# Performance work log

Hardware: AMD Instinct MI355X
Metric: run time of the kernel (lower is better)

Reference implementation:

```python
import jax, jax.numpy as jnp
import numpy as np

D = 768
N_ATOM = 1000 + 1   # num_atom_templates + 1
N_BOND = 300 + 1    # num_bond_templates + 1


def setup_inputs() -> dict:
    key = jax.random.key(0)
    k1, k2, k3, k4, k5 = jax.random.split(key, 5)
    scale = 1.0 / np.sqrt(D)
    return {
        "input_states": jax.random.normal(k1, (8, 256, D), dtype=jnp.float32),
        "Wa": jax.random.normal(k2, (N_ATOM, D), dtype=jnp.float32) * scale,
        "ba": jax.random.normal(k3, (N_ATOM,), dtype=jnp.float32) * 0.01,
        "Wb": jax.random.normal(k4, (N_BOND, 2 * D), dtype=jnp.float32) * scale,
        "bb": jax.random.normal(k5, (N_BOND,), dtype=jnp.float32) * 0.01,
    }


def reference(input_states, Wa, ba, Wb, bb):
    # Atom head: [B, L, n_a]
    atom_logits = jnp.einsum("bld,ad->bla", input_states, Wa) + ba

    # Bond head. Original math: linear(cat(x_i, x_j)) over all pairs (i, j).
    # Since Linear(cat(x_i, x_j)) = x_i @ W1.T + x_j @ W2.T + b with
    # W1 = Wb[:, :D], W2 = Wb[:, D:], we project once per token and
    # broadcast-add, avoiding the O(L^2 * 2D) concat intermediate.
    W1 = Wb[:, :D]
    W2 = Wb[:, D:]
    p1 = jnp.einsum("bld,nd->bln", input_states, W1)  # [B, L, n_b]
    p2 = jnp.einsum("bld,nd->bln", input_states, W2)  # [B, L, n_b]
    bond_logits = p1[:, :, None, :] + p2[:, None, :, :] + bb  # [B, L, L, n_b]

    return (atom_logits, bond_logits)
```

## Files before the change

kernel.cpp:

```cpp
#include <hip/hip_runtime.h>

#define DK      768
#define M_ROWS  2048
#define N_ATOM  1001
#define N_BOND  301
#define N_TOT   1603
#define N_PADR  1664
#define ATOM_ELEMS 2050048
#define P_ELEMS    616448
#define SLAB_F4    19264

typedef __attribute__((ext_vector_type(4))) float f32x4;
typedef __attribute__((ext_vector_type(8))) short bf16x8;

static __device__ __forceinline__ unsigned short f2bf(float f) {
    unsigned u = __float_as_uint(f);
    u += 0x7FFFu + ((u >> 16) & 1u);
    return (unsigned short)(u >> 16);
}

static __device__ __forceinline__ void gload_lds16(const void* g, void* l) {
    __builtin_amdgcn_global_load_lds(
        (const __attribute__((address_space(1))) unsigned*)g,
        (__attribute__((address_space(3))) unsigned*)l, 16, 0, 0);
}

__global__ __launch_bounds__(256) void pack_bf16(
    const float* __restrict__ x, const float* __restrict__ Wa,
    const float* __restrict__ Wb,
    ushort* __restrict__ xb, ushort* __restrict__ wcat)
{
    const int NX4 = (M_ROWS * DK) / 4;
    const int NW4 = (N_PADR * DK) / 4;
    int t = blockIdx.x * 256 + threadIdx.x;
    if (t < NX4) {
        float4 v = ((const float4*)x)[t];
        ushort4 o;
        o.x = f2bf(v.x); o.y = f2bf(v.y); o.z = f2bf(v.z); o.w = f2bf(v.w);
        ((ushort4*)xb)[t] = o;
    } else if (t < NX4 + NW4) {
        int u = t - NX4;
        int r = u / 192;
        int c = (u - r * 192) * 4;
        float4 v = make_float4(0.f, 0.f, 0.f, 0.f);
        if (r < N_ATOM) {
            v = *(const float4*)(Wa + (size_t)r * DK + c);
        } else if (r < N_TOT) {
            int q = r - N_ATOM;
            v = *(const float4*)(Wb + (size_t)(q >> 1) * (2 * DK) + (q & 1) * DK + c);
        }
        ushort4 o;
        o.x = f2bf(v.x); o.y = f2bf(v.y); o.z = f2bf(v.z); o.w = f2bf(v.w);
        ((ushort4*)wcat)[u] = o;
    }
}

__global__ __launch_bounds__(256) void gemm_mfma(
    const ushort* __restrict__ xb, const ushort* __restrict__ wcat,
    const float* __restrict__ ba, const float* __restrict__ bb,
    float* __restrict__ atom, float* __restrict__ p1, float* __restrict__ p2)
{
    __shared__ char As[8192];
    __shared__ char Bs[8192];

    const int tid  = threadIdx.x;
    const int lane = tid & 63;
    const int wid  = tid >> 6;
    const int wr   = wid >> 1;
    const int wc   = wid & 1;
    const int m0   = blockIdx.y * 64;
    const int n0   = blockIdx.x * 64;

    f32x4 acc[2][2] = {};

    const int lrow = lane >> 3;
    const int lcx  = ((lane & 7) ^ lrow) * 8;

    const ushort* Ag = xb   + (size_t)m0 * DK;
    const ushort* Bg = wcat + (size_t)n0 * DK;

    for (int k0 = 0; k0 < DK; k0 += 64) {
        __syncthreads();
        #pragma unroll
        for (int t = 0; t < 2; ++t) {
            const int s = wid + 4 * t;
            gload_lds16(Ag + (size_t)(s * 8 + lrow) * DK + k0 + lcx, As + s * 1024);
            gload_lds16(Bg + (size_t)(s * 8 + lrow) * DK + k0 + lcx, Bs + s * 1024);
        }
        __syncthreads();
        #pragma unroll
        for (int ks = 0; ks < 2; ++ks) {
            const int kc = ks * 4 + (lane >> 4);
            bf16x8 af[2], bfr[2];
            #pragma unroll
            for (int i = 0; i < 2; ++i) {
                int ra = wr * 32 + i * 16 + (lane & 15);
                af[i]  = *(const bf16x8*)(As + ra * 128 + ((kc ^ (ra & 7)) << 4));
                int rb = wc * 32 + i * 16 + (lane & 15);
                bfr[i] = *(const bf16x8*)(Bs + rb * 128 + ((kc ^ (rb & 7)) << 4));
            }
            #pragma unroll
            for (int i = 0; i < 2; ++i)
                #pragma unroll
                for (int j = 0; j < 2; ++j)
                    acc[i][j] = __builtin_amdgcn_mfma_f32_16x16x32_bf16(
                        af[i], bfr[j], acc[i][j], 0, 0, 0);
        }
    }

    #pragma unroll
    for (int i = 0; i < 2; ++i) {
        #pragma unroll
        for (int j = 0; j < 2; ++j) {
            #pragma unroll
            for (int reg = 0; reg < 4; ++reg) {
                int m = m0 + wr * 32 + i * 16 + (lane >> 4) * 4 + reg;
                int n = n0 + wc * 32 + j * 16 + (lane & 15);
                float v = acc[i][j][reg];
                if (n < N_ATOM) {
                    atom[(size_t)m * N_ATOM + n] = v + ba[n];
                } else if (n < N_TOT) {
                    int q = n - N_ATOM, rr = q >> 1;
                    if (q & 1) p2[(size_t)m * N_BOND + rr] = v + bb[rr];
                    else       p1[(size_t)m * N_BOND + rr] = v;
                }
            }
        }
    }
}

__global__ __launch_bounds__(256) void bond_bcast(
    const float* __restrict__ p1, const float* __restrict__ p2,
    f32x4* __restrict__ out)
{
    __shared__ float p1s[344];
    const int bi  = blockIdx.x;
    const int b   = bi >> 8;
    const int tid = threadIdx.x;

    for (int n = tid; n < N_BOND; n += 256)
        p1s[n + (n >> 3)] = p1[(size_t)bi * N_BOND + n];
    __syncthreads();

    const f32x4* p2f = (const f32x4*)(p2 + (size_t)(b << 8) * N_BOND);
    f32x4* of = out + (size_t)bi * SLAB_F4;

    int n = (4 * tid) % 301;
    for (int f = tid; f < SLAB_F4; f += 256) {
        f32x4 v = p2f[f];
        int n0 = n;
        int n1 = n + 1; if (n1 >= 301) n1 -= 301;
        int n2 = n + 2; if (n2 >= 301) n2 -= 301;
        int n3 = n + 3; if (n3 >= 301) n3 -= 301;
        v.x += p1s[n0 + (n0 >> 3)];
        v.y += p1s[n1 + (n1 >> 3)];
        v.z += p1s[n2 + (n2 >> 3)];
        v.w += p1s[n3 + (n3 >> 3)];
        of[f] = v;
        n += 121; if (n >= 301) n -= 301;
    }
}

extern "C" void kernel_launch(void* const* d_in, const int* in_sizes, int n_in,
                              void* d_out, int out_size, void* d_ws, size_t ws_size,
                              hipStream_t stream) {
    const float* x  = (const float*)d_in[0];
    const float* Wa = (const float*)d_in[1];
    const float* ba = (const float*)d_in[2];
    const float* Wb = (const float*)d_in[3];
    const float* bb = (const float*)d_in[4];

    float* out  = (float*)d_out;
    float* atom = out;
    float* bond = out + ATOM_ELEMS;

    ushort* xb   = (ushort*)d_ws;
    ushort* wcat = xb + (size_t)M_ROWS * DK;
    float*  p1   = (float*)(wcat + (size_t)N_PADR * DK);
    float*  p2   = p1 + P_ELEMS;

    pack_bf16<<<dim3(2784), dim3(256), 0, stream>>>(x, Wa, Wb, xb, wcat);

    gemm_mfma<<<dim3(N_PADR / 64, M_ROWS / 64), dim3(256), 0, stream>>>(
        xb, wcat, ba, bb, atom, p1, p2);

    bond_bcast<<<dim3(2048), dim3(256), 0, stream>>>(p1, p2, (f32x4*)bond);
}
```

Before: 183.0 us.

## Tile bond broadcast over 32x16 token pairs with both projections staged in LDS

The bond broadcast kernel now gives each block a 32-row by 16-column tile of (i, j) token pairs. It stages the matching p1 and p2 rows in shared memory, so the full per-batch p2 slab is no longer re-read from global/L2 for every output row. Output is written as coalesced scalar floats across 32 consecutive slab rows, and the grid shrinks to 1024 blocks. In exchange it uses about 58KB of LDS per block, which limits occupancy, and it drops the 16-byte vector stores in a kernel that is dominated by writes.

New measurement: 159.8 us. 1.15x faster.

```diff
diff --git a/kernel.cpp b/kernel.cpp
--- a/kernel.cpp
+++ b/kernel.cpp
@@ -8,7 +8,7 @@
 #define N_PADR  1664
 #define ATOM_ELEMS 2050048
 #define P_ELEMS    616448
-#define SLAB_F4    19264
+#define SLAB       77056
 
 typedef __attribute__((ext_vector_type(4))) float f32x4;
 typedef __attribute__((ext_vector_type(8))) short bf16x8;
@@ -131,33 +131,34 @@
 
 __global__ __launch_bounds__(256) void bond_bcast(
     const float* __restrict__ p1, const float* __restrict__ p2,
-    f32x4* __restrict__ out)
+    float* __restrict__ out)
 {
-    __shared__ float p1s[344];
-    const int bi  = blockIdx.x;
-    const int b   = bi >> 8;
+    __shared__ float p1s[32 * N_BOND];
+    __shared__ float p2s[16 * N_BOND];
+    const int blk = blockIdx.x;
+    const int b   = blk >> 7;
+    const int it  = (blk >> 4) & 7;
+    const int jt  = blk & 15;
     const int tid = threadIdx.x;
 
-    for (int n = tid; n < N_BOND; n += 256)
-        p1s[n + (n >> 3)] = p1[(size_t)bi * N_BOND + n];
+    const f32x4* p1g = (const f32x4*)(p1 + (size_t)(b * 256 + it * 32) * N_BOND);
+    const f32x4* p2g = (const f32x4*)(p2 + (size_t)(b * 256 + jt * 16) * N_BOND);
+    for (int k = tid; k < 2408; k += 256) ((f32x4*)p1s)[k] = p1g[k];
+    for (int k = tid; k < 1204; k += 256) ((f32x4*)p2s)[k] = p2g[k];
     __syncthreads();
 
-    const f32x4* p2f = (const f32x4*)(p2 + (size_t)(b << 8) * N_BOND);
-    f32x4* of = out + (size_t)bi * SLAB_F4;
-
-    int n = (4 * tid) % 301;
-    for (int f = tid; f < SLAB_F4; f += 256) {
-        f32x4 v = p2f[f];
-        int n0 = n;
-        int n1 = n + 1; if (n1 >= 301) n1 -= 301;
-        int n2 = n + 2; if (n2 >= 301) n2 -= 301;
-        int n3 = n + 3; if (n3 >= 301) n3 -= 301;
-        v.x += p1s[n0 + (n0 >> 3)];
-        v.y += p1s[n1 + (n1 >> 3)];
-        v.z += p1s[n2 + (n2 >> 3)];
-        v.w += p1s[n3 + (n3 >> 3)];
-        of[f] = v;
-        n += 121; if (n >= 301) n -= 301;
+    float* dst = out + (size_t)(b * 256 + it * 32) * SLAB + (size_t)(jt * 16) * N_BOND;
+    for (int i = 0; i < 32; ++i) {
+        const float* p1r = p1s + i * N_BOND;
+        float* o = dst + (size_t)i * SLAB;
+        int n = tid;
+        #pragma unroll
+        for (int k = 0; k < 19; ++k) {
+            int e = tid + k * 256;
+            if (k < 18 || e < 4816)
+                o[e] = p1r[n] + p2s[e];
+            n += 256; if (n >= N_BOND) n -= N_BOND;
+        }
     }
 }
 
@@ -184,5 +185,5 @@
     gemm_mfma<<<dim3(N_PADR / 64, M_ROWS / 64), dim3(256), 0, stream>>>(
         xb, wcat, ba, bb, atom, p1, p2);
 
-    bond_bcast<<<dim3(2048), dim3(256), 0, stream>>>(p1, p2, (f32x4*)bond);
+    bond_bcast<<<dim3(1024), dim3(256), 0, stream>>>(p1, p2, bond);
 }
```
